# Kernel optimization log

Measured on AMD Instinct MI355X. Metric: run time of the kernel, lower is better.

Reference implementation:

```python
import jax, jax.numpy as jnp
import numpy as np

H, I, B, S = 3200, 12800, 8, 1024  # InternViT-6B MLP dims


def setup_inputs() -> dict:
    key = jax.random.key(0)
    ks = jax.random.split(key, 8)
    # int8-valued activations/weights stored as int32 (harness dtype set)
    hidden_states = jax.random.randint(ks[0], (B, S, H), -127, 128, dtype=jnp.int32)
    scale = jax.random.uniform(ks[1], (B * S,), dtype=jnp.float32) * 1e-3 + 1e-5
    w1 = jax.random.randint(ks[2], (I, H), -127, 128, dtype=jnp.int32)
    w1_scale = jax.random.uniform(ks[3], (I,), dtype=jnp.float32) * 1e-3 + 1e-5
    b1 = jax.random.normal(ks[4], (I,), dtype=jnp.float32) * 0.02
    w2 = jax.random.randint(ks[5], (H, I), -127, 128, dtype=jnp.int32)
    w2_scale = jax.random.uniform(ks[6], (H,), dtype=jnp.float32) * 1e-3 + 1e-5
    b2 = jax.random.normal(ks[7], (H,), dtype=jnp.float32) * 0.02
    return {"hidden_states": hidden_states, "scale": scale, "w1": w1,
            "w1_scale": w1_scale, "b1": b1, "w2": w2, "w2_scale": w2_scale, "b2": b2}


def _w8a8_linear(x_q, x_scale, w_q, w_scale, b):
    # enough that fp32 matmul reproduces the exact integer accumulator to
    # within float32 rounding of the final sum.
    acc = jnp.matmul(x_q.astype(jnp.float32), w_q.astype(jnp.float32).T)  # [T, out]
    out = acc * x_scale[:, None] * w_scale[None, :] + b[None, :]
    return out.astype(jnp.float16)


def reference(hidden_states, scale, w1, w1_scale, b1, w2, w2_scale, b2):
    bsz, seq, hidden = hidden_states.shape
    x_q = hidden_states.reshape(-1, hidden)                 # [T, H] int8 values
    # fc1: W8A8 -> fp16 with dynamic per-token input scale
    fc1_out = _w8a8_linear(x_q, scale, w1, w1_scale, b1)    # [T, I] fp16
    # fused gelu_and_quant: exact GELU, then per-token dynamic int8 re-quant
    g = jax.nn.gelu(fc1_out.astype(jnp.float32), approximate=False)  # [T, I]
    new_scale = jnp.max(jnp.abs(g), axis=-1) / 127.0        # dynamic per-token scale
    act_q = jnp.clip(jnp.round(g / new_scale[:, None]), -127, 127)  # int8 values
    # fc2: W8A8 -> fp16
    out = _w8a8_linear(act_q, new_scale, w2, w2_scale, b2)  # [T, H] fp16
    return out
```

## Files before the change

kernel.cpp:

```cpp
#include <hip/hip_runtime.h>
#include <hip/hip_bf16.h>
#include <hip/hip_fp16.h>

#define T_DIM 8192
#define H_DIM 3200
#define I_DIM 12800

typedef int v4i __attribute__((ext_vector_type(4)));
typedef int v16i __attribute__((ext_vector_type(16)));
typedef _Float16 h8 __attribute__((ext_vector_type(8)));

__device__ __forceinline__ void gload16(const void* g, void* l) {
    __builtin_amdgcn_global_load_lds(
        (const __attribute__((address_space(1))) unsigned int*)g,
        (__attribute__((address_space(3))) unsigned int*)l, 16, 0, 0);
}

__global__ __launch_bounds__(256) void repack_kernel(const int* __restrict__ src,
                                                     unsigned int* __restrict__ dst,
                                                     long n4) {
    long i = (long)blockIdx.x * blockDim.x + threadIdx.x;
    long stride = (long)gridDim.x * blockDim.x;
    for (; i < n4; i += stride) {
        int4 v = ((const int4*)src)[i];
        dst[i] = (unsigned int)((v.x & 255) | ((v.y & 255) << 8) |
                                ((v.z & 255) << 16) | ((v.w & 255) << 24));
    }
}

template <int EPI>
__global__ __launch_bounds__(512, 2) void gemm_i8_32x32(
    const signed char* __restrict__ A, long strideA,
    const signed char* __restrict__ B, long strideB,
    int Ntrue, int K, int ldc,
    const float* __restrict__ rowscale, const float* __restrict__ colscale,
    const float* __restrict__ bias, void* __restrict__ Cout) {
    __shared__ signed char lds[131072];
    signed char* ldsA = lds;
    signed char* ldsB = lds + 65536;

    int bm, bn;
    {
        const int nwgx = gridDim.x;
        const int nwg = nwgx * gridDim.y;
        int id = blockIdx.x + nwgx * blockIdx.y;
        const int q = nwg >> 3, r = nwg & 7;
        const int x = id & 7, o = id >> 3;
        id = (x < r ? x * (q + 1) : r * (q + 1) + (x - r) * q) + o;
        bm = id % nwgx;
        bn = id / nwgx;
    }

    const int tid = threadIdx.x;
    const int lane = tid & 63, wid = tid >> 6;
    const int wr = wid >> 2, wc = wid & 3;
    const long Arow0 = (long)bm * 256;
    const long Bcol0 = (long)bn * 256;

    const int c0 = tid, c1 = tid + 512;
    const int r0 = c0 >> 2, r1_ = c1 >> 2;
    const int s0 = (((c0 & 3) ^ ((r0 >> 1) & 3)) << 4);
    const int s1 = (((c1 & 3) ^ ((r1_ >> 1) & 3)) << 4);
    const signed char* Ag0 = A + (Arow0 + r0) * strideA + s0;
    const signed char* Ag1 = A + (Arow0 + r1_) * strideA + s1;
    const signed char* Bg0 = B + (Bcol0 + r0) * strideB + s0;
    const signed char* Bg1 = B + (Bcol0 + r1_) * strideB + s1;
    const int d0 = c0 * 16, d1 = c1 * 16;

    const int NH = K >> 6;

#define STAGE_A(h)                                  \
    {                                               \
        const int hc_ = (h) < NH ? (h) : NH - 1;    \
        const long ko_ = (long)hc_ << 6;            \
        signed char* d_ = ldsA + (((h) & 3) << 14); \
        gload16(Ag0 + ko_, d_ + d0);                \
        gload16(Ag1 + ko_, d_ + d1);                \
    }
#define STAGE_B(h)                                  \
    {                                               \
        const int hc_ = (h) < NH ? (h) : NH - 1;    \
        const long ko_ = (long)hc_ << 6;            \
        signed char* d_ = ldsB + (((h) & 3) << 14); \
        gload16(Bg0 + ko_, d_ + d0);                \
        gload16(Bg1 + ko_, d_ + d1);                \
    }

    const int rl = lane & 31, qh = lane >> 5;
    const int x0 = ((qh ^ ((rl >> 1) & 3)) << 4);
    const int aoff = (wr * 128 + rl) * 64 + x0;
    const int boff = (wc * 64 + rl) * 64 + x0;

    v16i acc[4][2] = {};

    STAGE_A(0); STAGE_B(0); STAGE_A(1); STAGE_B(1); STAGE_A(2); STAGE_B(2);
    asm volatile("s_waitcnt vmcnt(8)");
    __builtin_amdgcn_s_barrier();

    for (int h = 0; h < NH; ++h) {
        const signed char* sA = ldsA + ((h & 3) << 14);
        const signed char* sB = ldsB + ((h & 3) << 14);
        v4i a0[4], a1[4], b0[2], b1[2];
#pragma unroll
        for (int m = 0; m < 4; ++m) {
            a0[m] = *(const v4i*)(sA + (aoff + m * 2048));
            a1[m] = *(const v4i*)(sA + ((aoff ^ 32) + m * 2048));
        }
#pragma unroll
        for (int n = 0; n < 2; ++n) {
            b0[n] = *(const v4i*)(sB + (boff + n * 2048));
            b1[n] = *(const v4i*)(sB + ((boff ^ 32) + n * 2048));
        }
        STAGE_A(h + 3);
        STAGE_B(h + 3);
        __builtin_amdgcn_s_barrier();
        asm volatile("s_waitcnt lgkmcnt(0)");
        __builtin_amdgcn_s_setprio(1);
#pragma unroll
        for (int m = 0; m < 4; ++m)
#pragma unroll
            for (int n = 0; n < 2; ++n)
                acc[m][n] = __builtin_amdgcn_mfma_i32_32x32x32_i8(
                    a0[m], b0[n], acc[m][n], 0, 0, 0);
#pragma unroll
        for (int m = 0; m < 4; ++m)
#pragma unroll
            for (int n = 0; n < 2; ++n)
                acc[m][n] = __builtin_amdgcn_mfma_i32_32x32x32_i8(
                    a1[m], b1[n], acc[m][n], 0, 0, 0);
        __builtin_amdgcn_s_setprio(0);
        asm volatile("s_waitcnt vmcnt(8)");
        __builtin_amdgcn_s_barrier();
    }

    const int row0 = bm * 256 + wr * 128;
    const int col0 = bn * 256 + wc * 64;
    const int rbase = 4 * qh;
#pragma unroll
    for (int m = 0; m < 4; ++m) {
#pragma unroll
        for (int n = 0; n < 2; ++n) {
            const int col = col0 + n * 32 + rl;
            if (col < Ntrue) {
                const float cs = colscale[col];
                const float bs = bias[col];
#pragma unroll
                for (int g = 0; g < 4; ++g) {
#pragma unroll
                    for (int rr = 0; rr < 4; ++rr) {
                        const int row = row0 + m * 32 + rbase + 8 * g + rr;
                        float v = (float)acc[m][n][g * 4 + rr];
                        v = __fmul_rn(v, rowscale[row]);
                        v = __fmul_rn(v, cs);
                        v = __fadd_rn(v, bs);
                        _Float16 hh = (_Float16)v;
                        const size_t idx = (size_t)row * ldc + col;
                        if (EPI == 0) ((_Float16*)Cout)[idx] = hh;
                        else ((float*)Cout)[idx] = (float)hh;
                    }
                }
            }
        }
    }
#undef STAGE_A
#undef STAGE_B
}

__global__ __launch_bounds__(256) void gelu_quant(_Float16* __restrict__ fc1,
                                                  float* __restrict__ nscale) {
    __shared__ float gbuf[I_DIM];
    __shared__ float wmax[4];
    const int tid = threadIdx.x, lane = tid & 63, wid = tid >> 6;
    const long t = blockIdx.x;
    const h8* row = (const h8*)(fc1 + t * I_DIM);
    float lmax = 0.f;
    for (int c = tid; c < I_DIM / 8; c += 256) {
        h8 v = row[c];
#pragma unroll
        for (int j = 0; j < 8; ++j) {
            float x = (float)v[j];
            float e = erff(__fdiv_rn(x, 1.41421356237309504880f));
            float g = __fmul_rn(__fmul_rn(0.5f, x), __fadd_rn(1.0f, e));
            gbuf[c * 8 + j] = g;
            lmax = fmaxf(lmax, fabsf(g));
        }
    }
#pragma unroll
    for (int off = 32; off; off >>= 1) lmax = fmaxf(lmax, __shfl_xor(lmax, off, 64));
    if (lane == 0) wmax[wid] = lmax;
    __syncthreads();
    const float gmax = fmaxf(fmaxf(wmax[0], wmax[1]), fmaxf(wmax[2], wmax[3]));
    const float ns = gmax / 127.0f;
    if (tid == 0) nscale[t] = ns;
    unsigned long long* out = (unsigned long long*)(fc1 + t * I_DIM);
    for (int c = tid; c < I_DIM / 8; c += 256) {
        unsigned long long pk = 0;
#pragma unroll
        for (int j = 0; j < 8; ++j) {
            float qv = rintf(__fdiv_rn(gbuf[c * 8 + j], ns));
            qv = fminf(fmaxf(qv, -127.f), 127.f);
            pk |= ((unsigned long long)(unsigned char)(signed char)(int)qv) << (8 * j);
        }
        out[c] = pk;
    }
}

extern "C" void kernel_launch(void* const* d_in, const int* in_sizes, int n_in,
                              void* d_out, int out_size, void* d_ws, size_t ws_size,
                              hipStream_t stream) {
    const int* hs = (const int*)d_in[0];
    const float* scale = (const float*)d_in[1];
    const int* w1 = (const int*)d_in[2];
    const float* w1s = (const float*)d_in[3];
    const float* b1 = (const float*)d_in[4];
    const int* w2 = (const int*)d_in[5];
    const float* w2s = (const float*)d_in[6];
    const float* b2 = (const float*)d_in[7];

    char* ws = (char*)d_ws;
    signed char* xq = (signed char*)ws;
    signed char* w1q = xq + (size_t)T_DIM * H_DIM;
    signed char* w2q = w1q + (size_t)I_DIM * H_DIM;
    _Float16* fc1h = (_Float16*)(w2q + (size_t)H_DIM * I_DIM);
    const size_t fixed = (size_t)T_DIM * H_DIM + 2 * (size_t)I_DIM * H_DIM;

    int nc = 1;
    while (nc < 16) {
        size_t need = fixed + ((size_t)T_DIM / nc) * I_DIM * 2 +
                      ((size_t)T_DIM / nc) * 4 + 256;
        if (need <= ws_size) break;
        nc <<= 1;
    }
    const int chunkT = T_DIM / nc;
    float* nscale = (float*)((char*)fc1h + (size_t)chunkT * I_DIM * 2);

    repack_kernel<<<2048, 256, 0, stream>>>(hs, (unsigned int*)xq, (long)T_DIM * H_DIM / 4);
    repack_kernel<<<2048, 256, 0, stream>>>(w1, (unsigned int*)w1q, (long)I_DIM * H_DIM / 4);
    repack_kernel<<<2048, 256, 0, stream>>>(w2, (unsigned int*)w2q, (long)H_DIM * I_DIM / 4);

    const int n2tiles = (H_DIM + 255) / 256;
    for (int c = 0; c < nc; ++c) {
        const int t0 = c * chunkT;
        gemm_i8_32x32<0><<<dim3(chunkT / 256, I_DIM / 256), 512, 0, stream>>>(
            xq + (size_t)t0 * H_DIM, (long)H_DIM, w1q, (long)H_DIM,
            I_DIM, H_DIM, I_DIM,
            scale + t0, w1s, b1, (void*)fc1h);
        gelu_quant<<<chunkT, 256, 0, stream>>>(fc1h, nscale);
        gemm_i8_32x32<1><<<dim3(chunkT / 256, n2tiles), 512, 0, stream>>>(
            (const signed char*)fc1h, (long)I_DIM * 2, w2q, (long)I_DIM,
            H_DIM, I_DIM, H_DIM,
            nscale, w2s, b2,
            (void*)((float*)d_out + (size_t)t0 * H_DIM));
    }
}
```

Measured before the change: 1.078 ms.

## Rework LDS tile layout for conflict-free MFMA fragment reads; drop workgroup remap

Changes how global 16-byte chunks map into LDS, so each 32-row block is stored as two 16-row halves with a new XOR swizzle. Fragment reads now use a fixed +1024 offset instead of an XOR on the address, which is meant to cut LDS bank conflicts on the ds_read path. It also removes the XCD-aware workgroup ID remapping and uses blockIdx directly, which may hurt L2 locality across the chiplets.

```diff
diff --git a/kernel.cpp b/kernel.cpp
--- a/kernel.cpp
+++ b/kernel.cpp
@@ -39,33 +39,32 @@
     signed char* ldsA = lds;
     signed char* ldsB = lds + 65536;
 
-    int bm, bn;
-    {
-        const int nwgx = gridDim.x;
-        const int nwg = nwgx * gridDim.y;
-        int id = blockIdx.x + nwgx * blockIdx.y;
-        const int q = nwg >> 3, r = nwg & 7;
-        const int x = id & 7, o = id >> 3;
-        id = (x < r ? x * (q + 1) : r * (q + 1) + (x - r) * q) + o;
-        bm = id % nwgx;
-        bn = id / nwgx;
-    }
-
     const int tid = threadIdx.x;
     const int lane = tid & 63, wid = tid >> 6;
     const int wr = wid >> 2, wc = wid & 3;
+    const int bm = blockIdx.x, bn = blockIdx.y;
     const long Arow0 = (long)bm * 256;
     const long Bcol0 = (long)bn * 256;
 
-    const int c0 = tid, c1 = tid + 512;
-    const int r0 = c0 >> 2, r1_ = c1 >> 2;
-    const int s0 = (((c0 & 3) ^ ((r0 >> 1) & 3)) << 4);
-    const int s1 = (((c1 & 3) ^ ((r1_ >> 1) & 3)) << 4);
-    const signed char* Ag0 = A + (Arow0 + r0) * strideA + s0;
-    const signed char* Ag1 = A + (Arow0 + r1_) * strideA + s1;
-    const signed char* Bg0 = B + (Bcol0 + r0) * strideB + s0;
-    const signed char* Bg1 = B + (Bcol0 + r1_) * strideB + s1;
-    const int d0 = c0 * 16, d1 = c1 * 16;
+    int g_row[2], g_cg[2];
+#pragma unroll
+    for (int u = 0; u < 2; ++u) {
+        const int ch = tid + (u << 9);
+        const int block = ch >> 7;
+        const int p = ch & 127;
+        const int half = (p >> 6) & 1;
+        const int p6 = p & 63;
+        const int r15 = p6 >> 2;
+        const int col = p6 & 3;
+        const int q = col ^ ((r15 >> 1) & 3);
+        g_row[u] = block * 32 + ((q & 1) << 4) + r15;
+        g_cg[u] = (half << 1) | (q >> 1);
+    }
+    const signed char* Ag0 = A + (Arow0 + g_row[0]) * strideA + g_cg[0] * 16;
+    const signed char* Ag1 = A + (Arow0 + g_row[1]) * strideA + g_cg[1] * 16;
+    const signed char* Bg0 = B + (Bcol0 + g_row[0]) * strideB + g_cg[0] * 16;
+    const signed char* Bg1 = B + (Bcol0 + g_row[1]) * strideB + g_cg[1] * 16;
+    const int d0 = tid * 16, d1 = (tid + 512) * 16;
 
     const int NH = K >> 6;
 
@@ -87,9 +86,11 @@
     }
 
     const int rl = lane & 31, qh = lane >> 5;
-    const int x0 = ((qh ^ ((rl >> 1) & 3)) << 4);
-    const int aoff = (wr * 128 + rl) * 64 + x0;
-    const int boff = (wc * 64 + rl) * 64 + x0;
+    const int r15 = rl & 15, qb = rl >> 4;
+    const int colr = ((qh << 1) | qb) ^ ((r15 >> 1) & 3);
+    const int roff = r15 * 64 + colr * 16;
+    const int aoff = (wr * 4) * 2048 + roff;
+    const int boff = (wc * 2) * 2048 + roff;
 
     v16i acc[4][2] = {};
 
@@ -103,13 +104,13 @@
         v4i a0[4], a1[4], b0[2], b1[2];
 #pragma unroll
         for (int m = 0; m < 4; ++m) {
-            a0[m] = *(const v4i*)(sA + (aoff + m * 2048));
-            a1[m] = *(const v4i*)(sA + ((aoff ^ 32) + m * 2048));
+            a0[m] = *(const v4i*)(sA + aoff + m * 2048);
+            a1[m] = *(const v4i*)(sA + aoff + m * 2048 + 1024);
         }
 #pragma unroll
         for (int n = 0; n < 2; ++n) {
-            b0[n] = *(const v4i*)(sB + (boff + n * 2048));
-            b1[n] = *(const v4i*)(sB + ((boff ^ 32) + n * 2048));
+            b0[n] = *(const v4i*)(sB + boff + n * 2048);
+            b1[n] = *(const v4i*)(sB + boff + n * 2048 + 1024);
         }
         STAGE_A(h + 3);
         STAGE_B(h + 3);
```

After: 1.110 ms. 3.0% more time.
